# Performance work log

Hardware: AMD Instinct MI355X
Metric: run time of the kernel (lower is better)

The kernel has to match this reference:

```python
import jax, jax.numpy as jnp
import numpy as np

N_NODES = 100000
N_EDGES = 1000000
D = 64  # input_size == hidden_size
N_CONVS = 6  # order: xz, hz, xr, hr, xh, hh


def setup_inputs() -> dict:
    key = jax.random.key(0)
    ks = jax.random.split(key, 12)
    s = 1.0 / np.sqrt(D)
    inp = {
        "x": jax.random.normal(ks[0], (N_NODES, D), dtype=jnp.float32),
        "h": jax.random.normal(ks[1], (N_NODES, D), dtype=jnp.float32),
        "edge_index": jax.random.randint(ks[2], (2, N_EDGES), 0, N_NODES, dtype=jnp.int32),
        # stacked params for the 6 TransformerConv layers: query/key/value/skip
        "Wq": jax.random.uniform(ks[3], (N_CONVS, D, D), jnp.float32, -s, s),
        "bq": jax.random.uniform(ks[4], (N_CONVS, D), jnp.float32, -s, s),
        "Wk": jax.random.uniform(ks[5], (N_CONVS, D, D), jnp.float32, -s, s),
        "bk": jax.random.uniform(ks[6], (N_CONVS, D), jnp.float32, -s, s),
        "Wv": jax.random.uniform(ks[7], (N_CONVS, D, D), jnp.float32, -s, s),
        "bv": jax.random.uniform(ks[8], (N_CONVS, D), jnp.float32, -s, s),
        "Ws": jax.random.uniform(ks[9], (N_CONVS, D, D), jnp.float32, -s, s),
        "bs": jax.random.uniform(ks[10], (N_CONVS, D), jnp.float32, -s, s),
    }
    return inp


def _transformer_conv(inp, src, dst, Wq, bq, Wk, bk, Wv, bv, Ws, bs):
    # PyG TransformerConv, heads=1, root_weight=True, beta=False
    q = inp @ Wq + bq  # [N, D]
    k = inp @ Wk + bk
    v = inp @ Wv + bv
    scores = jnp.sum(q[dst] * k[src], axis=-1) / jnp.sqrt(jnp.float32(D))  # [E]
    m = jax.ops.segment_max(scores, dst, num_segments=N_NODES)  # [N]
    m = jnp.where(jnp.isfinite(m), m, 0.0)
    e = jnp.exp(scores - m[dst])  # [E]
    denom = jax.ops.segment_sum(e, dst, num_segments=N_NODES)  # [N]
    alpha = e / (denom[dst] + 1e-16)  # [E]
    agg = jax.ops.segment_sum(alpha[:, None] * v[src], dst, num_segments=N_NODES)  # [N, D]
    return agg + inp @ Ws + bs  # skip connection (lin_skip)


def reference(x, h, edge_index, Wq, bq, Wk, bk, Wv, bv, Ws, bs):
    src, dst = edge_index[0], edge_index[1]

    def conv(i, inp):
        return _transformer_conv(inp, src, dst, Wq[i], bq[i], Wk[i], bk[i],
                                 Wv[i], bv[i], Ws[i], bs[i])

    z_g = jax.nn.sigmoid(conv(0, x) + conv(1, h))
    r_g = jax.nn.sigmoid(conv(2, x) + conv(3, h))
    h_tilde = jnp.tanh(conv(4, x) + conv(5, r_g * h))
    return z_g * h + (1.0 - z_g) * h_tilde
```

## Files before the change

### kernel.cpp

```cpp
#include <hip/hip_runtime.h>
#include <math.h>

#define N_NODES 100000
#define N_EDGES 1000000
#define D 64
#define N_CONVS 6
#define CAP 64
#define NDTOT (N_NODES * D)
#define NPART 8
#define CHUNK 4096

typedef __bf16 bf16x8 __attribute__((ext_vector_type(8)));
typedef float f32x4 __attribute__((ext_vector_type(4)));
typedef float f32x2 __attribute__((ext_vector_type(2)));

static __device__ __forceinline__ float hi2f(unsigned int d) {
    union { unsigned int i; float f; } c; c.i = d & 0xFFFF0000u; return c.f;
}
static __device__ __forceinline__ float lo2f(unsigned int d) {
    union { unsigned int i; float f; } c; c.i = d << 16; return c.f;
}
static __device__ __forceinline__ unsigned short f2bf(float f) {
    union { float f; unsigned int i; } c; c.f = f;
    unsigned int x = c.i;
    unsigned int r = (x + 0x7fffu + ((x >> 16) & 1u)) >> 16;
    return (unsigned short)r;
}


#if __has_builtin(__builtin_amdgcn_cvt_pk_f32_fp8) && __has_builtin(__builtin_amdgcn_cvt_pk_fp8_f32)
#define HW_FP8 1
#endif

#ifndef HW_FP8
static __device__ __forceinline__ float dec1(unsigned int b) {
    union { unsigned int i; float f; } c;
    c.i = ((b & 0x80u) << 24) | ((b & 0x7fu) << 20);
    return c.f * 0x1p+120f;
}
static __device__ __forceinline__ unsigned int enc1(float f) {
    union { float f; unsigned int i; } c; c.f = f;
    unsigned int s = (c.i >> 24) & 0x80u;
    float a = fabsf(f);
    a = fminf(a, 448.0f);
    c.f = a * 0x1p-120f;
    unsigned int u = c.i;
    unsigned int bits = (u + 0x7FFFFu + ((u >> 20) & 1u)) >> 20;
    if (bits > 0x7Eu) bits = 0x7Eu;
    return s | bits;
}
#endif

static __device__ __forceinline__ void dec8(unsigned int lo, unsigned int hi, float* f) {
#ifdef HW_FP8
    f32x2 p0 = __builtin_amdgcn_cvt_pk_f32_fp8(lo, false);
    f32x2 p1 = __builtin_amdgcn_cvt_pk_f32_fp8(lo, true);
    f32x2 p2 = __builtin_amdgcn_cvt_pk_f32_fp8(hi, false);
    f32x2 p3 = __builtin_amdgcn_cvt_pk_f32_fp8(hi, true);
    f[0] = p0[0]; f[1] = p0[1]; f[2] = p1[0]; f[3] = p1[1];
    f[4] = p2[0]; f[5] = p2[1]; f[6] = p3[0]; f[7] = p3[1];
#else
#pragma unroll
    for (int i = 0; i < 4; ++i) f[i] = dec1((lo >> (8 * i)) & 0xFFu);
#pragma unroll
    for (int i = 0; i < 4; ++i) f[4 + i] = dec1((hi >> (8 * i)) & 0xFFu);
#endif
}

static __device__ __forceinline__ unsigned int enc4(float a, float b, float c2, float d) {
#ifdef HW_FP8
    int r = 0;
    r = __builtin_amdgcn_cvt_pk_fp8_f32(a, b, r, false);
    r = __builtin_amdgcn_cvt_pk_fp8_f32(c2, d, r, true);
    return (unsigned int)r;
#else
    return enc1(a) | (enc1(b) << 8) | (enc1(c2) << 16) | (enc1(d) << 24);
#endif
}


__global__ void fill_cap_part(const int* __restrict__ src, const int* __restrict__ dst,
                              int E, int* __restrict__ cnt, int* __restrict__ colIdx) {
    const int part = blockIdx.x & (NPART - 1);
    const int base = (blockIdx.x >> 3) * CHUNK;
    const int lo = part * (N_NODES / NPART);
    const int hi = lo + (N_NODES / NPART);
#pragma unroll
    for (int it = 0; it < CHUNK / 256; ++it) {
        int e = base + it * 256 + (int)threadIdx.x;
        if (e < E) {
            int d = dst[e];
            if (d >= lo && d < hi) {
                int slot = atomicAdd(&cnt[d], 1);
                if (slot < CAP) colIdx[(size_t)d * CAP + slot] = src[e];
            }
        }
    }
}


__global__ void prep_all(const float* __restrict__ x, const float* __restrict__ h,
                         unsigned short* __restrict__ xb, unsigned short* __restrict__ hb,
                         const float* __restrict__ Wq, const float* __restrict__ Wk,
                         const float* __restrict__ Wv, const float* __restrict__ Ws,
                         const float* __restrict__ bq, const float* __restrict__ bk,
                         const float* __restrict__ bv, const float* __restrict__ bs,
                         unsigned short* __restrict__ WT, float* __restrict__ ball,
                         int nCvt) {
    int b = blockIdx.x;
    if (b < nCvt) {
        int i = (b * 256 + threadIdx.x) * 4;
        if (i < NDTOT) {
            float4 fx = *(const float4*)&x[i];
            float4 fh = *(const float4*)&h[i];
            ushort4 ux, uh;
            ux.x = f2bf(fx.x); ux.y = f2bf(fx.y); ux.z = f2bf(fx.z); ux.w = f2bf(fx.w);
            uh.x = f2bf(fh.x); uh.y = f2bf(fh.y); uh.z = f2bf(fh.z); uh.w = f2bf(fh.w);
            *(ushort4*)&xb[i] = ux;
            *(ushort4*)&hb[i] = uh;
        }
    } else {
        int idx = (b - nCvt) * 256 + threadIdx.x;
        if (idx >= N_CONVS * 256 * 64) return;
        int conv = idx >> 14;
        int rem = idx & 16383;
        int n = rem >> 6, kk = rem & 63;
        int mat = n >> 6, c = n & 63;
        const float* W = mat == 0 ? Wq : mat == 1 ? Wk : mat == 2 ? Wv : Ws;
        WT[idx] = f2bf(W[conv * 4096 + kk * 64 + c]);
        if (kk == 0) {
            const float* B = mat == 0 ? bq : mat == 1 ? bk : mat == 2 ? bv : bs;
            ball[conv * 256 + n] = B[conv * 64 + c];
        }
    }
}


static __device__ __forceinline__ void gemm_pair_body(
    const unsigned short* __restrict__ XA, const unsigned short* __restrict__ XB, int N,
    const unsigned short* __restrict__ WTA, const unsigned short* __restrict__ WTB,
    const float* __restrict__ ballA, const float* __restrict__ ballB,
    unsigned short* __restrict__ qboth, unsigned char* __restrict__ kv8,
    float* __restrict__ sk)
{
    __shared__ __align__(16) unsigned short XLA[64][72];
    __shared__ __align__(16) unsigned short XLB[64][72];
    __shared__ __align__(16) float SKIP[64][68];

    const int tid = threadIdx.x;
    const int base = blockIdx.x * 64;
    const int lane = tid & 63;
    const int wave = tid >> 6;
    const int conv = wave >> 2;
    const int mat = wave & 3;

    {
        int r = tid >> 3, cc = (tid & 7) * 8;
        uint4 va = {0u,0u,0u,0u}, vb = {0u,0u,0u,0u};
        if (base + r < N) {
            va = *(const uint4*)&XA[(size_t)(base + r) * D + cc];
            vb = *(const uint4*)&XB[(size_t)(base + r) * D + cc];
        }
        *(uint4*)&XLA[r][cc] = va;
        *(uint4*)&XLB[r][cc] = vb;
    }
    __syncthreads();

    const int l15 = lane & 15;
    const int lhi = lane >> 4;
    const int n0 = mat * 64;
    const unsigned short* WT = conv ? WTB : WTA;
    const float* ball = conv ? ballB : ballA;

    bf16x8 Wf[4][2];
#pragma unroll
    for (int ni = 0; ni < 4; ++ni)
#pragma unroll
        for (int ks = 0; ks < 2; ++ks)
            Wf[ni][ks] = *(const bf16x8*)&WT[(size_t)(n0 + ni * 16 + l15) * D + lhi * 8 + ks * 32];

    bf16x8 Xf[4][2];
#pragma unroll
    for (int mi = 0; mi < 4; ++mi)
#pragma unroll
        for (int ks = 0; ks < 2; ++ks)
            Xf[mi][ks] = conv ? *(const bf16x8*)&XLB[mi * 16 + l15][lhi * 8 + ks * 32]
                              : *(const bf16x8*)&XLA[mi * 16 + l15][lhi * 8 + ks * 32];

    f32x4 acc[4][4];
#pragma unroll
    for (int ni = 0; ni < 4; ++ni) {
        const float4 b4 = *(const float4*)&ball[n0 + ni * 16 + lhi * 4];
#pragma unroll
        for (int mi = 0; mi < 4; ++mi) {
            f32x4 t;
            t[0] = b4.x; t[1] = b4.y; t[2] = b4.z; t[3] = b4.w;
            acc[mi][ni] = t;
        }
    }

#pragma unroll
    for (int ks = 0; ks < 2; ++ks)
#pragma unroll
        for (int mi = 0; mi < 4; ++mi)
#pragma unroll
            for (int ni = 0; ni < 4; ++ni)
                acc[mi][ni] = __builtin_amdgcn_mfma_f32_16x16x32_bf16(
                    Wf[ni][ks], Xf[mi][ks], acc[mi][ni], 0, 0, 0);

    if (mat == 0) {
        unsigned short* outb = qboth + conv * 64;
#pragma unroll
        for (int mi = 0; mi < 4; ++mi) {
            int row = base + mi * 16 + l15;
            if (row < N) {
#pragma unroll
                for (int ni = 0; ni < 4; ++ni) {
                    int col = ni * 16 + lhi * 4;
                    ushort4 u;
                    u.x = f2bf(acc[mi][ni][0]); u.y = f2bf(acc[mi][ni][1]);
                    u.z = f2bf(acc[mi][ni][2]); u.w = f2bf(acc[mi][ni][3]);
                    *(ushort4*)&outb[(size_t)row * 128 + col] = u;
                }
            }
        }
    } else if (mat < 3) {
        unsigned char* outb = kv8 + conv * 128 + (mat == 2 ? 64 : 0);
#pragma unroll
        for (int mi = 0; mi < 4; ++mi) {
            int row = base + mi * 16 + l15;
            if (row < N) {
#pragma unroll
                for (int ni = 0; ni < 4; ++ni) {
                    int col = ni * 16 + lhi * 4;
                    unsigned int r = enc4(acc[mi][ni][0], acc[mi][ni][1],
                                          acc[mi][ni][2], acc[mi][ni][3]);
                    *(unsigned int*)&outb[(size_t)row * 256 + col] = r;
                }
            }
        }
    } else if (conv == 0) {
#pragma unroll
        for (int mi = 0; mi < 4; ++mi)
#pragma unroll
            for (int ni = 0; ni < 4; ++ni)
                *(f32x4*)&SKIP[mi * 16 + l15][ni * 16 + lhi * 4] = acc[mi][ni];
    }
    __syncthreads();
    if (mat == 3 && conv == 1) {
#pragma unroll
        for (int mi = 0; mi < 4; ++mi) {
            int row = base + mi * 16 + l15;
            if (row < N) {
#pragma unroll
                for (int ni = 0; ni < 4; ++ni) {
                    int col = ni * 16 + lhi * 4;
                    const f32x4 s4 = *(const f32x4*)&SKIP[mi * 16 + l15][col];
                    float4 r4;
                    r4.x = acc[mi][ni][0] + s4[0];
                    r4.y = acc[mi][ni][1] + s4[1];
                    r4.z = acc[mi][ni][2] + s4[2];
                    r4.w = acc[mi][ni][3] + s4[3];
                    *(float4*)&sk[(size_t)row * 64 + col] = r4;
                }
            }
        }
    }
}

__global__ __launch_bounds__(512) void gemm_pair(
    const unsigned short* __restrict__ XA, const unsigned short* __restrict__ XB, int N,
    const unsigned short* __restrict__ WTA, const unsigned short* __restrict__ WTB,
    const float* __restrict__ ballA, const float* __restrict__ ballB,
    unsigned short* __restrict__ qboth, unsigned char* __restrict__ kv8,
    float* __restrict__ sk)
{
    gemm_pair_body(XA, XB, N, WTA, WTB, ballA, ballB, qboth, kv8, sk);
}


__global__ __launch_bounds__(256) void edge_attn2(
    const int* __restrict__ cnt, const int* __restrict__ colIdx,
    const unsigned short* __restrict__ qboth, const unsigned char* __restrict__ kv8,
    float* __restrict__ tgt, int N)
{
    const int tid = threadIdx.x;
    const int node = blockIdx.x * 32 + (tid >> 3);
    if (node >= N) return;
    const int t = tid & 7;

    int deg = cnt[node];
    if (deg > CAP) deg = CAP;

    const float SC = 0.18033688f;
    const uint4 qa4 = *(const uint4*)&qboth[(size_t)node * 128 + t * 8];
    const uint4 qb4 = *(const uint4*)&qboth[(size_t)node * 128 + 64 + t * 8];
    float qa[8], qb[8];
    qa[0] = lo2f(qa4.x) * SC; qa[1] = hi2f(qa4.x) * SC;
    qa[2] = lo2f(qa4.y) * SC; qa[3] = hi2f(qa4.y) * SC;
    qa[4] = lo2f(qa4.z) * SC; qa[5] = hi2f(qa4.z) * SC;
    qa[6] = lo2f(qa4.w) * SC; qa[7] = hi2f(qa4.w) * SC;
    qb[0] = lo2f(qb4.x) * SC; qb[1] = hi2f(qb4.x) * SC;
    qb[2] = lo2f(qb4.y) * SC; qb[3] = hi2f(qb4.y) * SC;
    qb[4] = lo2f(qb4.z) * SC; qb[5] = hi2f(qb4.z) * SC;
    qb[6] = lo2f(qb4.w) * SC; qb[7] = hi2f(qb4.w) * SC;

    const size_t rowbase = (size_t)node * CAP;

    float l0 = 0.0f, l1 = 0.0f;
    float a0[8], a1[8];
#pragma unroll
    for (int i = 0; i < 8; ++i) { a0[i] = 0.0f; a1[i] = 0.0f; }

    for (int j = 0; j < deg; j += 2) {
        const bool v2 = (j + 1) < deg;
        const int s1 = colIdx[rowbase + j];
        const int s2 = colIdx[rowbase + (v2 ? j + 1 : j)];
        const unsigned char* p1 = kv8 + (size_t)s1 * 256 + t * 8;
        const unsigned char* p2 = kv8 + (size_t)s2 * 256 + t * 8;
        const uint2 ka1 = *(const uint2*)p1;
        const uint2 va1 = *(const uint2*)(p1 + 64);
        const uint2 kb1 = *(const uint2*)(p1 + 128);
        const uint2 vb1 = *(const uint2*)(p1 + 192);
        const uint2 ka2 = *(const uint2*)p2;
        const uint2 va2 = *(const uint2*)(p2 + 64);
        const uint2 kb2 = *(const uint2*)(p2 + 128);
        const uint2 vb2 = *(const uint2*)(p2 + 192);

        float kf[8];
        dec8(ka1.x, ka1.y, kf);
        float pa1 = qa[0]*kf[0] + qa[1]*kf[1] + qa[2]*kf[2] + qa[3]*kf[3]
                  + qa[4]*kf[4] + qa[5]*kf[5] + qa[6]*kf[6] + qa[7]*kf[7];
        dec8(kb1.x, kb1.y, kf);
        float pb1 = qb[0]*kf[0] + qb[1]*kf[1] + qb[2]*kf[2] + qb[3]*kf[3]
                  + qb[4]*kf[4] + qb[5]*kf[5] + qb[6]*kf[6] + qb[7]*kf[7];
        dec8(ka2.x, ka2.y, kf);
        float pa2 = qa[0]*kf[0] + qa[1]*kf[1] + qa[2]*kf[2] + qa[3]*kf[3]
                  + qa[4]*kf[4] + qa[5]*kf[5] + qa[6]*kf[6] + qa[7]*kf[7];
        dec8(kb2.x, kb2.y, kf);
        float pb2 = qb[0]*kf[0] + qb[1]*kf[1] + qb[2]*kf[2] + qb[3]*kf[3]
                  + qb[4]*kf[4] + qb[5]*kf[5] + qb[6]*kf[6] + qb[7]*kf[7];

        pa1 += __shfl_xor(pa1, 1); pb1 += __shfl_xor(pb1, 1);
        pa2 += __shfl_xor(pa2, 1); pb2 += __shfl_xor(pb2, 1);
        pa1 += __shfl_xor(pa1, 2); pb1 += __shfl_xor(pb1, 2);
        pa2 += __shfl_xor(pa2, 2); pb2 += __shfl_xor(pb2, 2);
        pa1 += __shfl_xor(pa1, 4); pb1 += __shfl_xor(pb1, 4);
        pa2 += __shfl_xor(pa2, 4); pb2 += __shfl_xor(pb2, 4);

        const float w01 = exp2f(pa1);
        const float w11 = exp2f(pb1);
        const float w02 = v2 ? exp2f(pa2) : 0.0f;
        const float w12 = v2 ? exp2f(pb2) : 0.0f;
        l0 += w01 + w02; l1 += w11 + w12;

        float vf1[8], vf2[8];
        dec8(va1.x, va1.y, vf1);
        dec8(va2.x, va2.y, vf2);
#pragma unroll
        for (int i = 0; i < 8; ++i) a0[i] += w01 * vf1[i] + w02 * vf2[i];
        dec8(vb1.x, vb1.y, vf1);
        dec8(vb2.x, vb2.y, vf2);
#pragma unroll
        for (int i = 0; i < 8; ++i) a1[i] += w11 * vf1[i] + w12 * vf2[i];
    }

    const float inv0 = 1.0f / (l0 + 1e-16f);
    const float inv1 = 1.0f / (l1 + 1e-16f);
    float* pout = &tgt[(size_t)node * 64 + t * 8];
    float4 o1 = *(float4*)pout;
    float4 o2 = *(float4*)(pout + 4);
    o1.x += a0[0] * inv0 + a1[0] * inv1;
    o1.y += a0[1] * inv0 + a1[1] * inv1;
    o1.z += a0[2] * inv0 + a1[2] * inv1;
    o1.w += a0[3] * inv0 + a1[3] * inv1;
    o2.x += a0[4] * inv0 + a1[4] * inv1;
    o2.y += a0[5] * inv0 + a1[5] * inv1;
    o2.z += a0[6] * inv0 + a1[6] * inv1;
    o2.w += a0[7] * inv0 + a1[7] * inv1;
    *(float4*)pout = o1;
    *(float4*)(pout + 4) = o2;
}


__global__ void rh_kernel(const float* __restrict__ rpre, const float* __restrict__ h,
                          unsigned short* __restrict__ rhb, int n) {
    int i = (blockIdx.x * 256 + threadIdx.x) * 4;
    if (i < n) {
        float4 rp = *(const float4*)&rpre[i];
        float4 hh = *(const float4*)&h[i];
        ushort4 o;
        o.x = f2bf(hh.x / (1.0f + __expf(-rp.x)));
        o.y = f2bf(hh.y / (1.0f + __expf(-rp.y)));
        o.z = f2bf(hh.z / (1.0f + __expf(-rp.z)));
        o.w = f2bf(hh.w / (1.0f + __expf(-rp.w)));
        *(ushort4*)&rhb[i] = o;
    }
}

__global__ void final_kernel(const float* __restrict__ zpre, const float* __restrict__ h,
                             const float* __restrict__ c45, float* __restrict__ out, int n) {
    int i = (blockIdx.x * 256 + threadIdx.x) * 4;
    if (i < n) {
        float4 zp = *(const float4*)&zpre[i];
        float4 hh = *(const float4*)&h[i];
        float4 cc = *(const float4*)&c45[i];
        float4 r;
        float z0 = 1.0f / (1.0f + __expf(-zp.x));
        float z1 = 1.0f / (1.0f + __expf(-zp.y));
        float z2 = 1.0f / (1.0f + __expf(-zp.z));
        float z3 = 1.0f / (1.0f + __expf(-zp.w));
        r.x = z0 * hh.x + (1.0f - z0) * tanhf(cc.x);
        r.y = z1 * hh.y + (1.0f - z1) * tanhf(cc.y);
        r.z = z2 * hh.z + (1.0f - z2) * tanhf(cc.z);
        r.w = z3 * hh.w + (1.0f - z3) * tanhf(cc.w);
        *(float4*)&out[i] = r;
    }
}


extern "C" void kernel_launch(void* const* d_in, const int* in_sizes, int n_in,
                              void* d_out, int out_size, void* d_ws, size_t ws_size,
                              hipStream_t stream) {
    const int N = N_NODES, E = N_EDGES;
    const float* x  = (const float*)d_in[0];
    const float* h  = (const float*)d_in[1];
    const int*  ei  = (const int*)d_in[2];
    const float* Wq = (const float*)d_in[3];
    const float* bq = (const float*)d_in[4];
    const float* Wk = (const float*)d_in[5];
    const float* bk = (const float*)d_in[6];
    const float* Wv = (const float*)d_in[7];
    const float* bv = (const float*)d_in[8];
    const float* Ws = (const float*)d_in[9];
    const float* bs = (const float*)d_in[10];
    float* out = (float*)d_out;

    const int* src = ei;
    const int* dst = ei + E;

    char* w = (char*)d_ws;
    int* cnt    = (int*)w;
    int* colIdx = cnt + N;
    size_t intWords = (size_t)N + (size_t)N * CAP;
    char* p = w + ((intWords * 4 + 255) & ~(size_t)255);

    const size_t ND = (size_t)N * D;
    float* zpre = (float*)p;            p += ND * 4;
    float* rpre = (float*)p;            p += ND * 4;
    float* c45  = (float*)p;            p += ND * 4;
    float* ball = (float*)p;            p += N_CONVS * 256 * 4;
    unsigned short* xb    = (unsigned short*)p; p += ND * 2;
    unsigned short* hb    = (unsigned short*)p; p += ND * 2;
    unsigned short* rhb   = (unsigned short*)p; p += ND * 2;
    unsigned short* qboth = (unsigned short*)p; p += ND * 2 * 2;
    unsigned char*  kv8   = (unsigned char*)p;  p += (size_t)N_NODES * 256;
    unsigned short* WT    = (unsigned short*)p; p += (size_t)N_CONVS * 256 * 64 * 2;

    const int NB_CVT = (int)(ND / 4 / 256);
    const int NB_PP = (N_CONVS * 256 * 64 + 255) / 256;
    const int NB_GEMM = (N + 63) / 64;
    const int NB_FILL = ((E + CHUNK - 1) / CHUNK) * NPART;
    const int NB_ATTN = (N + 31) / 32;
    const int NB_EW = (int)(ND / 4 / 256);

    prep_all<<<NB_CVT + NB_PP, 256, 0, stream>>>(x, h, xb, hb, Wq, Wk, Wv, Ws,
                                                 bq, bk, bv, bs, WT, ball, NB_CVT);
    hipMemsetAsync(cnt, 0, (size_t)N * sizeof(int), stream);
    fill_cap_part<<<NB_FILL, 256, 0, stream>>>(src, dst, E, cnt, colIdx);

#define WTc(i) (WT + (size_t)(i) * 256 * 64)
#define BLc(i) (ball + (size_t)(i) * 256)

    gemm_pair<<<NB_GEMM, 512, 0, stream>>>(
        xb, hb, N, WTc(0), WTc(1), BLc(0), BLc(1), qboth, kv8, zpre);
    edge_attn2<<<NB_ATTN, 256, 0, stream>>>(cnt, colIdx, qboth, kv8, zpre, N);

    gemm_pair<<<NB_GEMM, 512, 0, stream>>>(
        xb, hb, N, WTc(2), WTc(3), BLc(2), BLc(3), qboth, kv8, rpre);
    edge_attn2<<<NB_ATTN, 256, 0, stream>>>(cnt, colIdx, qboth, kv8, rpre, N);

    rh_kernel<<<NB_EW, 256, 0, stream>>>(rpre, h, rhb, (int)ND);
    gemm_pair<<<NB_GEMM, 512, 0, stream>>>(
        xb, rhb, N, WTc(4), WTc(5), BLc(4), BLc(5), qboth, kv8, c45);
    edge_attn2<<<NB_ATTN, 256, 0, stream>>>(cnt, colIdx, qboth, kv8, c45, N);

    final_kernel<<<NB_EW, 256, 0, stream>>>(zpre, h, c45, out, (int)ND);

#undef WTc
#undef BLc
}
```

Measured before the change: 375.9 us.

## Fuse z/r gate GEMMs into one kernel and fold elementwise ops into attention epilogues

New measurement: 357.8 us. 1.05x faster.

```diff
diff --git a/kernel.cpp b/kernel.cpp
--- a/kernel.cpp
+++ b/kernel.cpp
@@ -136,7 +136,148 @@
 }
 
 
-static __device__ __forceinline__ void gemm_pair_body(
+__global__ __launch_bounds__(512) void gemm_quad(
+    const unsigned short* __restrict__ XA, const unsigned short* __restrict__ XB, int N,
+    const unsigned short* __restrict__ WT4, const float* __restrict__ ball4,
+    unsigned short* __restrict__ qboth2,
+    unsigned char* __restrict__ kv8a,
+    unsigned char* __restrict__ kv8b,
+    float* __restrict__ zskip, float* __restrict__ rskip)
+{
+    __shared__ __align__(16) unsigned short XLA[64][72];
+    __shared__ __align__(16) unsigned short XLB[64][72];
+    __shared__ __align__(16) float SKIP[64][68];
+
+    const int tid = threadIdx.x;
+    const int base = blockIdx.x * 64;
+    const int lane = tid & 63;
+    const int wave = tid >> 6;
+    const int cSel = wave >> 2;
+    const int mat = wave & 3;
+
+    {
+        int r = tid >> 3, cc = (tid & 7) * 8;
+        uint4 va = {0u,0u,0u,0u}, vb = {0u,0u,0u,0u};
+        if (base + r < N) {
+            va = *(const uint4*)&XA[(size_t)(base + r) * D + cc];
+            vb = *(const uint4*)&XB[(size_t)(base + r) * D + cc];
+        }
+        *(uint4*)&XLA[r][cc] = va;
+        *(uint4*)&XLB[r][cc] = vb;
+    }
+    __syncthreads();
+
+    const int l15 = lane & 15;
+    const int lhi = lane >> 4;
+    const int n0 = mat * 64;
+
+    bf16x8 Xf[4][2];
+#pragma unroll
+    for (int mi = 0; mi < 4; ++mi)
+#pragma unroll
+        for (int ks = 0; ks < 2; ++ks)
+            Xf[mi][ks] = cSel ? *(const bf16x8*)&XLB[mi * 16 + l15][lhi * 8 + ks * 32]
+                              : *(const bf16x8*)&XLA[mi * 16 + l15][lhi * 8 + ks * 32];
+
+#pragma unroll
+    for (int pp = 0; pp < 2; ++pp) {
+        const int conv = pp * 2 + cSel;
+        const unsigned short* WT = WT4 + (size_t)conv * 256 * 64;
+        const float* ball = ball4 + conv * 256;
+
+        bf16x8 Wf[4][2];
+#pragma unroll
+        for (int ni = 0; ni < 4; ++ni)
+#pragma unroll
+            for (int ks = 0; ks < 2; ++ks)
+                Wf[ni][ks] = *(const bf16x8*)&WT[(size_t)(n0 + ni * 16 + l15) * D + lhi * 8 + ks * 32];
+
+        f32x4 acc[4][4];
+#pragma unroll
+        for (int ni = 0; ni < 4; ++ni) {
+            const float4 b4 = *(const float4*)&ball[n0 + ni * 16 + lhi * 4];
+#pragma unroll
+            for (int mi = 0; mi < 4; ++mi) {
+                f32x4 t;
+                t[0] = b4.x; t[1] = b4.y; t[2] = b4.z; t[3] = b4.w;
+                acc[mi][ni] = t;
+            }
+        }
+
+#pragma unroll
+        for (int ks = 0; ks < 2; ++ks)
+#pragma unroll
+            for (int mi = 0; mi < 4; ++mi)
+#pragma unroll
+                for (int ni = 0; ni < 4; ++ni)
+                    acc[mi][ni] = __builtin_amdgcn_mfma_f32_16x16x32_bf16(
+                        Wf[ni][ks], Xf[mi][ks], acc[mi][ni], 0, 0, 0);
+
+        if (mat == 0) {
+            unsigned short* outb = qboth2 + pp * 128 + cSel * 64;
+#pragma unroll
+            for (int mi = 0; mi < 4; ++mi) {
+                int row = base + mi * 16 + l15;
+                if (row < N) {
+#pragma unroll
+                    for (int ni = 0; ni < 4; ++ni) {
+                        int col = ni * 16 + lhi * 4;
+                        ushort4 u;
+                        u.x = f2bf(acc[mi][ni][0]); u.y = f2bf(acc[mi][ni][1]);
+                        u.z = f2bf(acc[mi][ni][2]); u.w = f2bf(acc[mi][ni][3]);
+                        *(ushort4*)&outb[(size_t)row * 256 + col] = u;
+                    }
+                }
+            }
+        } else if (mat < 3) {
+            unsigned char* outb = (pp ? kv8b : kv8a) + cSel * 128 + (mat == 2 ? 64 : 0);
+#pragma unroll
+            for (int mi = 0; mi < 4; ++mi) {
+                int row = base + mi * 16 + l15;
+                if (row < N) {
+#pragma unroll
+                    for (int ni = 0; ni < 4; ++ni) {
+                        int col = ni * 16 + lhi * 4;
+                        unsigned int r = enc4(acc[mi][ni][0], acc[mi][ni][1],
+                                              acc[mi][ni][2], acc[mi][ni][3]);
+                        *(unsigned int*)&outb[(size_t)row * 256 + col] = r;
+                    }
+                }
+            }
+        } else if (cSel == 0) {
+#pragma unroll
+            for (int mi = 0; mi < 4; ++mi)
+#pragma unroll
+                for (int ni = 0; ni < 4; ++ni)
+                    *(f32x4*)&SKIP[mi * 16 + l15][ni * 16 + lhi * 4] = acc[mi][ni];
+        }
+        __syncthreads();
+        if (mat == 3 && cSel == 1) {
+            float* skout = pp ? rskip : zskip;
+#pragma unroll
+            for (int mi = 0; mi < 4; ++mi) {
+                int row = base + mi * 16 + l15;
+                if (row < N) {
+#pragma unroll
+                    for (int ni = 0; ni < 4; ++ni) {
+                        int col = ni * 16 + lhi * 4;
+                        const f32x4 s4 = *(const f32x4*)&SKIP[mi * 16 + l15][col];
+                        float4 r4;
+                        r4.x = acc[mi][ni][0] + s4[0];
+                        r4.y = acc[mi][ni][1] + s4[1];
+                        r4.z = acc[mi][ni][2] + s4[2];
+                        r4.w = acc[mi][ni][3] + s4[3];
+                        *(float4*)&skout[(size_t)row * 64 + col] = r4;
+                    }
+                }
+            }
+        }
+        __syncthreads();
+    }
+}
+
+
+__global__ __launch_bounds__(512) void gemm_pair(
     const unsigned short* __restrict__ XA, const unsigned short* __restrict__ XB, int N,
     const unsigned short* __restrict__ WTA, const unsigned short* __restrict__ WTB,
     const float* __restrict__ ballA, const float* __restrict__ ballB,
@@ -268,21 +409,15 @@
     }
 }
 
-__global__ __launch_bounds__(512) void gemm_pair(
-    const unsigned short* __restrict__ XA, const unsigned short* __restrict__ XB, int N,
-    const unsigned short* __restrict__ WTA, const unsigned short* __restrict__ WTB,
-    const float* __restrict__ ballA, const float* __restrict__ ballB,
-    unsigned short* __restrict__ qboth, unsigned char* __restrict__ kv8,
-    float* __restrict__ sk)
-{
-    gemm_pair_body(XA, XB, N, WTA, WTB, ballA, ballB, qboth, kv8, sk);
-}
-
-
-__global__ __launch_bounds__(256) void edge_attn2(
+
+template<int MODE>
+__global__ __launch_bounds__(256) void edge_attn_t(
     const int* __restrict__ cnt, const int* __restrict__ colIdx,
-    const unsigned short* __restrict__ qboth, const unsigned char* __restrict__ kv8,
-    float* __restrict__ tgt, int N)
+    const unsigned short* __restrict__ qptr, int qstride,
+    const unsigned char* __restrict__ kv8,
+    const float* __restrict__ skip, const float* __restrict__ zpre,
+    const float* __restrict__ hfull,
+    float* __restrict__ tgt, unsigned short* __restrict__ rhb, int N)
 {
     const int tid = threadIdx.x;
     const int node = blockIdx.x * 32 + (tid >> 3);
@@ -293,8 +428,8 @@
     if (deg > CAP) deg = CAP;
 
     const float SC = 0.18033688f;
-    const uint4 qa4 = *(const uint4*)&qboth[(size_t)node * 128 + t * 8];
-    const uint4 qb4 = *(const uint4*)&qboth[(size_t)node * 128 + 64 + t * 8];
+    const uint4 qa4 = *(const uint4*)&qptr[(size_t)node * qstride + t * 8];
+    const uint4 qb4 = *(const uint4*)&qptr[(size_t)node * qstride + 64 + t * 8];
     float qa[8], qb[8];
     qa[0] = lo2f(qa4.x) * SC; qa[1] = hi2f(qa4.x) * SC;
     qa[2] = lo2f(qa4.y) * SC; qa[3] = hi2f(qa4.y) * SC;
@@ -367,54 +502,55 @@
 
     const float inv0 = 1.0f / (l0 + 1e-16f);
     const float inv1 = 1.0f / (l1 + 1e-16f);
-    float* pout = &tgt[(size_t)node * 64 + t * 8];
-    float4 o1 = *(float4*)pout;
-    float4 o2 = *(float4*)(pout + 4);
-    o1.x += a0[0] * inv0 + a1[0] * inv1;
-    o1.y += a0[1] * inv0 + a1[1] * inv1;
-    o1.z += a0[2] * inv0 + a1[2] * inv1;
-    o1.w += a0[3] * inv0 + a1[3] * inv1;
-    o2.x += a0[4] * inv0 + a1[4] * inv1;
-    o2.y += a0[5] * inv0 + a1[5] * inv1;
-    o2.z += a0[6] * inv0 + a1[6] * inv1;
-    o2.w += a0[7] * inv0 + a1[7] * inv1;
-    *(float4*)pout = o1;
-    *(float4*)(pout + 4) = o2;
-}
-
-
-__global__ void rh_kernel(const float* __restrict__ rpre, const float* __restrict__ h,
-                          unsigned short* __restrict__ rhb, int n) {
-    int i = (blockIdx.x * 256 + threadIdx.x) * 4;
-    if (i < n) {
-        float4 rp = *(const float4*)&rpre[i];
-        float4 hh = *(const float4*)&h[i];
-        ushort4 o;
-        o.x = f2bf(hh.x / (1.0f + __expf(-rp.x)));
-        o.y = f2bf(hh.y / (1.0f + __expf(-rp.y)));
-        o.z = f2bf(hh.z / (1.0f + __expf(-rp.z)));
-        o.w = f2bf(hh.w / (1.0f + __expf(-rp.w)));
-        *(ushort4*)&rhb[i] = o;
-    }
-}
-
-__global__ void final_kernel(const float* __restrict__ zpre, const float* __restrict__ h,
-                             const float* __restrict__ c45, float* __restrict__ out, int n) {
-    int i = (blockIdx.x * 256 + threadIdx.x) * 4;
-    if (i < n) {
-        float4 zp = *(const float4*)&zpre[i];
-        float4 hh = *(const float4*)&h[i];
-        float4 cc = *(const float4*)&c45[i];
-        float4 r;
-        float z0 = 1.0f / (1.0f + __expf(-zp.x));
-        float z1 = 1.0f / (1.0f + __expf(-zp.y));
-        float z2 = 1.0f / (1.0f + __expf(-zp.z));
-        float z3 = 1.0f / (1.0f + __expf(-zp.w));
-        r.x = z0 * hh.x + (1.0f - z0) * tanhf(cc.x);
-        r.y = z1 * hh.y + (1.0f - z1) * tanhf(cc.y);
-        r.z = z2 * hh.z + (1.0f - z2) * tanhf(cc.z);
-        r.w = z3 * hh.w + (1.0f - z3) * tanhf(cc.w);
-        *(float4*)&out[i] = r;
+    float o[8];
+#pragma unroll
+    for (int i = 0; i < 8; ++i) o[i] = a0[i] * inv0 + a1[i] * inv1;
+
+    const size_t off = (size_t)node * 64 + t * 8;
+
+    if (MODE == 0) {
+        float* pout = &tgt[off];
+        float4 o1 = *(float4*)pout;
+        float4 o2 = *(float4*)(pout + 4);
+        o1.x += o[0]; o1.y += o[1]; o1.z += o[2]; o1.w += o[3];
+        o2.x += o[4]; o2.y += o[5]; o2.z += o[6]; o2.w += o[7];
+        *(float4*)pout = o1;
+        *(float4*)(pout + 4) = o2;
+    } else if (MODE == 1) {
+        const float4 s1 = *(const float4*)&skip[off];
+        const float4 s2 = *(const float4*)&skip[off + 4];
+        const float4 h1 = *(const float4*)&hfull[off];
+        const float4 h2 = *(const float4*)&hfull[off + 4];
+        ushort4 u1, u2;
+        u1.x = f2bf(h1.x / (1.0f + __expf(-(s1.x + o[0]))));
+        u1.y = f2bf(h1.y / (1.0f + __expf(-(s1.y + o[1]))));
+        u1.z = f2bf(h1.z / (1.0f + __expf(-(s1.z + o[2]))));
+        u1.w = f2bf(h1.w / (1.0f + __expf(-(s1.w + o[3]))));
+        u2.x = f2bf(h2.x / (1.0f + __expf(-(s2.x + o[4]))));
+        u2.y = f2bf(h2.y / (1.0f + __expf(-(s2.y + o[5]))));
+        u2.z = f2bf(h2.z / (1.0f + __expf(-(s2.z + o[6]))));
+        u2.w = f2bf(h2.w / (1.0f + __expf(-(s2.w + o[7]))));
+        *(ushort4*)&rhb[off] = u1;
+        *(ushort4*)&rhb[off + 4] = u2;
+    } else {
+        const float4 s1 = *(const float4*)&skip[off];
+        const float4 s2 = *(const float4*)&skip[off + 4];
+        const float4 z1 = *(const float4*)&zpre[off];
+        const float4 z2 = *(const float4*)&zpre[off + 4];
+        const float4 h1 = *(const float4*)&hfull[off];
+        const float4 h2 = *(const float4*)&hfull[off + 4];
+        float4 r1, r2;
+        float zz;
+        zz = 1.0f / (1.0f + __expf(-z1.x)); r1.x = zz * h1.x + (1.0f - zz) * tanhf(s1.x + o[0]);
+        zz = 1.0f / (1.0f + __expf(-z1.y)); r1.y = zz * h1.y + (1.0f - zz) * tanhf(s1.y + o[1]);
+        zz = 1.0f / (1.0f + __expf(-z1.z)); r1.z = zz * h1.z + (1.0f - zz) * tanhf(s1.z + o[2]);
+        zz = 1.0f / (1.0f + __expf(-z1.w)); r1.w = zz * h1.w + (1.0f - zz) * tanhf(s1.w + o[3]);
+        zz = 1.0f / (1.0f + __expf(-z2.x)); r2.x = zz * h2.x + (1.0f - zz) * tanhf(s2.x + o[4]);
+        zz = 1.0f / (1.0f + __expf(-z2.y)); r2.y = zz * h2.y + (1.0f - zz) * tanhf(s2.y + o[5]);
+        zz = 1.0f / (1.0f + __expf(-z2.z)); r2.z = zz * h2.z + (1.0f - zz) * tanhf(s2.z + o[6]);
+        zz = 1.0f / (1.0f + __expf(-z2.w)); r2.w = zz * h2.w + (1.0f - zz) * tanhf(s2.w + o[7]);
+        *(float4*)&tgt[off] = r1;
+        *(float4*)&tgt[off + 4] = r2;
     }
 }
 
@@ -446,23 +582,23 @@
     char* p = w + ((intWords * 4 + 255) & ~(size_t)255);
 
     const size_t ND = (size_t)N * D;
-    float* zpre = (float*)p;            p += ND * 4;
-    float* rpre = (float*)p;            p += ND * 4;
-    float* c45  = (float*)p;            p += ND * 4;
-    float* ball = (float*)p;            p += N_CONVS * 256 * 4;
-    unsigned short* xb    = (unsigned short*)p; p += ND * 2;
-    unsigned short* hb    = (unsigned short*)p; p += ND * 2;
-    unsigned short* rhb   = (unsigned short*)p; p += ND * 2;
-    unsigned short* qboth = (unsigned short*)p; p += ND * 2 * 2;
-    unsigned char*  kv8   = (unsigned char*)p;  p += (size_t)N_NODES * 256;
-    unsigned short* WT    = (unsigned short*)p; p += (size_t)N_CONVS * 256 * 64 * 2;
+    float* zpre  = (float*)p;            p += ND * 4;
+    float* rskip = (float*)p;            p += ND * 4;
+    float* ball  = (float*)p;            p += N_CONVS * 256 * 4;
+    unsigned short* xb     = (unsigned short*)p; p += ND * 2;
+    unsigned short* hb     = (unsigned short*)p; p += ND * 2;
+    unsigned short* rhb    = (unsigned short*)p; p += ND * 2;
+    unsigned short* qboth2 = (unsigned short*)p; p += ND * 2 * 4;
+    unsigned char*  kv8a   = (unsigned char*)p;  p += (size_t)N_NODES * 256;
+    unsigned char*  kv8b   = (unsigned char*)p;  p += (size_t)N_NODES * 256;
+    unsigned short* WT     = (unsigned short*)p; p += (size_t)N_CONVS * 256 * 64 * 2;
+    float* cskip = rskip;
 
     const int NB_CVT = (int)(ND / 4 / 256);
     const int NB_PP = (N_CONVS * 256 * 64 + 255) / 256;
     const int NB_GEMM = (N + 63) / 64;
     const int NB_FILL = ((E + CHUNK - 1) / CHUNK) * NPART;
     const int NB_ATTN = (N + 31) / 32;
-    const int NB_EW = (int)(ND / 4 / 256);
 
     prep_all<<<NB_CVT + NB_PP, 256, 0, stream>>>(x, h, xb, hb, Wq, Wk, Wv, Ws,
                                                  bq, bk, bv, bs, WT, ball, NB_CVT);
@@ -472,20 +608,20 @@
 #define WTc(i) (WT + (size_t)(i) * 256 * 64)
 #define BLc(i) (ball + (size_t)(i) * 256)
 
+    gemm_quad<<<NB_GEMM, 512, 0, stream>>>(
+        xb, hb, N, WT, ball, qboth2, kv8a, kv8b, zpre, rskip);
+
+    edge_attn_t<0><<<NB_ATTN, 256, 0, stream>>>(
+        cnt, colIdx, qboth2, 256, kv8a, nullptr, nullptr, nullptr, zpre, nullptr, N);
+
+    edge_attn_t<1><<<NB_ATTN, 256, 0, stream>>>(
+        cnt, colIdx, qboth2 + 128, 256, kv8b, rskip, nullptr, h, nullptr, rhb, N);
+
     gemm_pair<<<NB_GEMM, 512, 0, stream>>>(
-        xb, hb, N, WTc(0), WTc(1), BLc(0), BLc(1), qboth, kv8, zpre);
-    edge_attn2<<<NB_ATTN, 256, 0, stream>>>(cnt, colIdx, qboth, kv8, zpre, N);
-
-    gemm_pair<<<NB_GEMM, 512, 0, stream>>>(
-        xb, hb, N, WTc(2), WTc(3), BLc(2), BLc(3), qboth, kv8, rpre);
-    edge_attn2<<<NB_ATTN, 256, 0, stream>>>(cnt, colIdx, qboth, kv8, rpre, N);
-
-    rh_kernel<<<NB_EW, 256, 0, stream>>>(rpre, h, rhb, (int)ND);
-    gemm_pair<<<NB_GEMM, 512, 0, stream>>>(
-        xb, rhb, N, WTc(4), WTc(5), BLc(4), BLc(5), qboth, kv8, c45);
-    edge_attn2<<<NB_ATTN, 256, 0, stream>>>(cnt, colIdx, qboth, kv8, c45, N);
-
-    final_kernel<<<NB_EW, 256, 0, stream>>>(zpre, h, c45, out, (int)ND);
+        xb, rhb, N, WTc(4), WTc(5), BLc(4), BLc(5), qboth2, kv8a, cskip);
+
+    edge_attn_t<2><<<NB_ATTN, 256, 0, stream>>>(
+        cnt, colIdx, qboth2, 128, kv8a, cskip, zpre, h, out, nullptr, N);
 
 #undef WTc
 #undef BLc
```
